# Optimization experiments

Hardware: AMD Instinct MI355X
Metric: run time of the kernel (lower is better)

Reference implementation:

```python
import jax, jax.numpy as jnp
import numpy as np

B, T = 16, 2048
OBS_DIM, ACT_DIM, HIDDEN = 64, 16, 512


def setup_inputs() -> dict:
    key = jax.random.key(0)
    ks = jax.random.split(key, 6)
    n = lambda k, shape, scale: (jax.random.normal(k, shape, dtype=jnp.float32) * scale)
    return {
        "obs": n(ks[0], (B, T, OBS_DIM), 1.0),
        "act": n(ks[1], (B, T, ACT_DIM), 1.0),
        "W_e": n(ks[2], (HIDDEN, OBS_DIM + ACT_DIM), 0.05),   # embed Linear weight
        "b_e": jnp.zeros((HIDDEN,), jnp.float32),             # embed Linear bias
        "a_raw": n(ks[3], (HIDDEN,), 0.5),                    # diagonal decay (pre-tanh)
        "W_B": n(ks[4], (HIDDEN, HIDDEN), 0.02),              # B Linear weight (no bias)
        "W_out": n(ks[5], (OBS_DIM, HIDDEN), 0.04),           # out Linear weight
        "b_out": jnp.zeros((OBS_DIM,), jnp.float32),          # out Linear bias
    }


def reference(obs, act, W_e, b_e, a_raw, W_B, W_out, b_out):
    # x: [B, T, obs+act]
    x = jnp.concatenate([obs, act], axis=-1)
    # embed: Linear + ReLU, batched over all timesteps -> u: [B, T, H]
    u = jax.nn.relu(jnp.einsum('btd,hd->bth', x, W_e) + b_e)
    # B projection batched over all t (the per-step matmul in the torch loop)
    v = jnp.einsum('bth,gh->btg', u, W_B)  # [B, T, H]
    a = jnp.tanh(a_raw)  # [H]
    # Diagonal linear recurrence s_t = a * s_{t-1} + v_t, s_0 starting from zeros,
    # realized as a parallel (log-depth) associative scan over (decay, input) pairs.
    A = jnp.broadcast_to(a, v.shape)
    def combine(c1, c2):
        a1, b1 = c1
        a2, b2 = c2
        return (a1 * a2, a2 * b1 + b2)
    _, s = jax.lax.associative_scan(combine, (A, v), axis=1)  # s: [B, T, H]
    # out projection per step -> preds: [B, T, obs_dim]
    return jnp.einsum('bth,oh->bto', s, W_out) + b_out
```

## Files before the change

kernel.cpp:

```cpp
#include <hip/hip_runtime.h>
#include <hip/hip_bf16.h>

#define B_    16
#define T_    2048
#define H_    512
#define BT_   32768
#define DIN   80
#define DPAD  128
#define L_    64
#define C_    32
#define O_    64
#define NCHUNK (BT_ / L_)

typedef __attribute__((ext_vector_type(8))) short short8;
typedef __attribute__((ext_vector_type(4))) float f32x4;
typedef __attribute__((ext_vector_type(4))) float float4v;

__device__ __forceinline__ float bf2f(unsigned short u) {
  union { unsigned int i; float f; } x; x.i = ((unsigned int)u) << 16; return x.f;
}
__device__ __forceinline__ unsigned short f2bf(float f) {
  union { float f; unsigned int i; } x; x.f = f;
  unsigned int r = x.i + 0x7fffu + ((x.i >> 16) & 1u);
  return (unsigned short)(r >> 16);
}

__global__ __launch_bounds__(512) void gemm_bproj(
    const unsigned short* __restrict__ A, const unsigned short* __restrict__ Bt,
    unsigned short* __restrict__ Cb,
    const float* __restrict__ powa,
    float* __restrict__ e)
{
  constexpr int NT = 8;
  __shared__ __align__(16) unsigned char lds[131072];

  const int tid  = threadIdx.x;
  const int lane = tid & 63;
  const int wid  = tid >> 6;
  const int wr   = wid >> 2;
  const int wc   = wid & 3;
  const int cl   = lane & 15;
  const int kgrp = lane >> 4;
  const int rg   = kgrp * 4;

  const int X  = (int)blockIdx.x & 7;
  const int j  = (int)blockIdx.x >> 3;
  const int mt = X * 16 + (j >> 1);
  const int nt = j & 1;
  const int row0 = mt * 256, col0 = nt * 256;

  auto stageA = [&](int q, int buf) {
    const int k0 = q * 64;
    #pragma unroll
    for (int r = 0; r < 4; ++r) {
      const int o   = r * 8192 + tid * 16;
      const int row = o >> 7;
      const int c16 = (o >> 4) & 7;
      const int kk  = (c16 ^ (row & 7)) << 3;
      __builtin_amdgcn_global_load_lds(
          (const __attribute__((address_space(1))) void*)
              (A + (size_t)(row0 + row) * H_ + k0 + kk),
          (__attribute__((address_space(3))) void*)(lds + buf * 65536 + o),
          16, 0, 0);
    }
  };
  auto stageB_round = [&](int q, int buf, int r) {
    const int k0 = q * 64;
    const int o   = r * 8192 + tid * 16;
    const int col = o >> 7;
    const int c16 = (o >> 4) & 7;
    const int kk  = (c16 ^ (col & 7)) << 3;
    __builtin_amdgcn_global_load_lds(
        (const __attribute__((address_space(1))) void*)
            (Bt + (size_t)(col0 + col) * H_ + k0 + kk),
        (__attribute__((address_space(3))) void*)(lds + buf * 65536 + 32768 + o),
        16, 0, 0);
  };

  f32x4 acc[8][4];
  #pragma unroll
  for (int m = 0; m < 8; ++m)
    #pragma unroll
    for (int n = 0; n < 4; ++n) acc[m][n] = f32x4{0.f, 0.f, 0.f, 0.f};

  stageA(0, 0);
  #pragma unroll
  for (int r = 0; r < 4; ++r) stageB_round(0, 0, r);
  #pragma unroll
  for (int r = 0; r < 4; ++r) stageB_round(1, 1, r);
  asm volatile("s_waitcnt vmcnt(4)" ::: "memory");
  __builtin_amdgcn_sched_barrier(0);
  __builtin_amdgcn_s_barrier();

  for (int q = 0; q < NT; ++q) {
    const int cur = q & 1;
    const unsigned char* bufp = lds + cur * 65536;

    if (q + 1 < NT) stageA(q + 1, cur ^ 1);

    short8 bfr[4][2];
    #pragma unroll
    for (int n = 0; n < 4; ++n) {
      const int col = wc * 64 + n * 16 + cl;
      #pragma unroll
      for (int ks = 0; ks < 2; ++ks)
        bfr[n][ks] = *(const short8*)(bufp + 32768 + col * 128 +
                                      ((((ks << 2) + kgrp) ^ (col & 7)) << 4));
    }
    asm volatile("s_waitcnt lgkmcnt(0)" ::: "memory");
    __builtin_amdgcn_sched_barrier(0);
    __builtin_amdgcn_s_barrier();

    __builtin_amdgcn_s_setprio(1);
    #pragma unroll
    for (int g = 0; g < 4; ++g) {
      if (q + 2 < NT) stageB_round(q + 2, cur, g);
      short8 af[2][2];
      #pragma unroll
      for (int mm = 0; mm < 2; ++mm) {
        const int row = wr * 128 + (g * 2 + mm) * 16 + cl;
        #pragma unroll
        for (int ks = 0; ks < 2; ++ks)
          af[mm][ks] = *(const short8*)(bufp + row * 128 +
                                        ((((ks << 2) + kgrp) ^ (row & 7)) << 4));
      }
      #pragma unroll
      for (int ks = 0; ks < 2; ++ks)
        #pragma unroll
        for (int mm = 0; mm < 2; ++mm)
          #pragma unroll
          for (int n = 0; n < 4; ++n)
            acc[g * 2 + mm][n] = __builtin_amdgcn_mfma_f32_16x16x32_bf16(
                af[mm][ks], bfr[n][ks], acc[g * 2 + mm][n], 0, 0, 0);
    }
    __builtin_amdgcn_s_setprio(0);

    if (q + 2 < NT) {
      asm volatile("s_waitcnt vmcnt(4)" ::: "memory");
    } else if (q + 1 < NT) {
      asm volatile("s_waitcnt vmcnt(0)" ::: "memory");
    }
    __builtin_amdgcn_sched_barrier(0);
    __builtin_amdgcn_s_barrier();
  }

  #pragma unroll
  for (int m = 0; m < 8; ++m) {
    #pragma unroll
    for (int n = 0; n < 4; ++n) {
      const int gc = col0 + wc * 64 + n * 16 + cl;
      #pragma unroll
      for (int e2 = 0; e2 < 4; ++e2) {
        const int gr = row0 + wr * 128 + m * 16 + rg + e2;
        Cb[(size_t)gr * H_ + gc] = f2bf(acc[m][n][e2]);
      }
    }
  }

  #pragma unroll
  for (int c = 0; c < 2; ++c) {
    const int chunk = ((row0 + wr * 128) >> 6) + c;
    #pragma unroll
    for (int n = 0; n < 4; ++n) {
      const int h = col0 + wc * 64 + n * 16 + cl;
      const float a16 = powa[15 * H_ + h];
      float ep = 0.f;
      #pragma unroll
      for (int e2 = 0; e2 < 4; ++e2) {
        const int k = 15 - rg - e2;
        const float wk = (k == 0) ? 1.f : powa[(size_t)(k - 1) * H_ + h];
        float hsum = acc[c * 4 + 0][n][e2];
        hsum = fmaf(hsum, a16, acc[c * 4 + 1][n][e2]);
        hsum = fmaf(hsum, a16, acc[c * 4 + 2][n][e2]);
        hsum = fmaf(hsum, a16, acc[c * 4 + 3][n][e2]);
        ep = fmaf(wk, hsum, ep);
      }
      ep += __shfl_xor(ep, 16);
      ep += __shfl_xor(ep, 32);
      if (kgrp == 0)
        e[(size_t)chunk * H_ + h] = ep;
    }
  }
}

__global__ __launch_bounds__(512) void embed_gemm(
    const float* __restrict__ obs, const float* __restrict__ act,
    const unsigned short* __restrict__ Web,
    const float* __restrict__ b_e,
    unsigned short* __restrict__ u)
{
  __shared__ __align__(16) unsigned char lds[131072];

  const int tid  = threadIdx.x;
  const int lane = tid & 63;
  const int wid  = tid >> 6;
  const int wr   = wid >> 2;
  const int wc   = wid & 3;
  const int cl   = lane & 15;
  const int kgrp = lane >> 4;
  const int rg   = kgrp * 4;

  const int X  = (int)blockIdx.x & 7;
  const int j  = (int)blockIdx.x >> 3;
  const int mt = X * 16 + (j >> 1);
  const int nt = j & 1;
  const int row0 = mt * 256, col0 = nt * 256;

  {
    const int row  = tid >> 1;
    const int half = tid & 1;
    {
      const float4v* src = (const float4v*)(obs + (size_t)(row0 + row) * 64 + half * 32);
      float f[32];
      #pragma unroll
      for (int i = 0; i < 8; ++i) {
        const float4v t4 = src[i];
        f[i*4+0]=t4[0]; f[i*4+1]=t4[1]; f[i*4+2]=t4[2]; f[i*4+3]=t4[3];
      }
      #pragma unroll
      for (int cc = 0; cc < 4; ++cc) {
        short8 o8;
        #pragma unroll
        for (int jj = 0; jj < 8; ++jj) o8[jj] = (short)f2bf(f[cc*8+jj]);
        const int c16 = half * 4 + cc;
        *(short8*)(lds + row * 128 + ((c16 ^ (row & 7)) << 4)) = o8;
      }
    }
    {
      short8 z8;
      #pragma unroll
      for (int jj = 0; jj < 8; ++jj) z8[jj] = 0;
      if (half == 0) {
        const float4v* asrc = (const float4v*)(act + (size_t)(row0 + row) * 16);
        float g[16];
        #pragma unroll
        for (int i = 0; i < 4; ++i) {
          const float4v t4 = asrc[i];
          g[i*4+0]=t4[0]; g[i*4+1]=t4[1]; g[i*4+2]=t4[2]; g[i*4+3]=t4[3];
        }
        #pragma unroll
        for (int cc = 0; cc < 2; ++cc) {
          short8 o8;
          #pragma unroll
          for (int jj = 0; jj < 8; ++jj) o8[jj] = (short)f2bf(g[cc*8+jj]);
          *(short8*)(lds + 65536 + row * 128 + ((cc ^ (row & 7)) << 4)) = o8;
        }
        #pragma unroll
        for (int cc = 2; cc < 4; ++cc)
          *(short8*)(lds + 65536 + row * 128 + ((cc ^ (row & 7)) << 4)) = z8;
      } else {
        #pragma unroll
        for (int cc = 4; cc < 8; ++cc)
          *(short8*)(lds + 65536 + row * 128 + ((cc ^ (row & 7)) << 4)) = z8;
      }
    }
  }
  #pragma unroll
  for (int q = 0; q < 2; ++q) {
    #pragma unroll
    for (int r = 0; r < 4; ++r) {
      const int o   = r * 8192 + tid * 16;
      const int col = o >> 7;
      const int c16 = (o >> 4) & 7;
      const int kk  = (c16 ^ (col & 7)) << 3;
      __builtin_amdgcn_global_load_lds(
          (const __attribute__((address_space(1))) void*)
              (Web + (size_t)(col0 + col) * DPAD + q * 64 + kk),
          (__attribute__((address_space(3))) void*)(lds + q * 65536 + 32768 + o),
          16, 0, 0);
    }
  }
  __syncthreads();

  f32x4 acc[8][4];
  #pragma unroll
  for (int m = 0; m < 8; ++m)
    #pragma unroll
    for (int n = 0; n < 4; ++n) acc[m][n] = f32x4{0.f, 0.f, 0.f, 0.f};

  #pragma unroll
  for (int q = 0; q < 2; ++q) {
    const unsigned char* bufp = lds + q * 65536;
    short8 bfr[4][2];
    #pragma unroll
    for (int n = 0; n < 4; ++n) {
      const int col = wc * 64 + n * 16 + cl;
      #pragma unroll
      for (int ks = 0; ks < 2; ++ks)
        bfr[n][ks] = *(const short8*)(bufp + 32768 + col * 128 +
                                      ((((ks << 2) + kgrp) ^ (col & 7)) << 4));
    }
    #pragma unroll
    for (int g = 0; g < 4; ++g) {
      short8 af[2][2];
      #pragma unroll
      for (int mm = 0; mm < 2; ++mm) {
        const int row = wr * 128 + (g * 2 + mm) * 16 + cl;
        #pragma unroll
        for (int ks = 0; ks < 2; ++ks)
          af[mm][ks] = *(const short8*)(bufp + row * 128 +
                                        ((((ks << 2) + kgrp) ^ (row & 7)) << 4));
      }
      #pragma unroll
      for (int ks = 0; ks < 2; ++ks)
        #pragma unroll
        for (int mm = 0; mm < 2; ++mm)
          #pragma unroll
          for (int n = 0; n < 4; ++n)
            acc[g * 2 + mm][n] = __builtin_amdgcn_mfma_f32_16x16x32_bf16(
                af[mm][ks], bfr[n][ks], acc[g * 2 + mm][n], 0, 0, 0);
    }
  }

  #pragma unroll
  for (int m = 0; m < 8; ++m) {
    #pragma unroll
    for (int n = 0; n < 4; ++n) {
      const int gc = col0 + wc * 64 + n * 16 + cl;
      const float be = b_e[gc];
      #pragma unroll
      for (int e2 = 0; e2 < 4; ++e2) {
        const int gr = row0 + wr * 128 + m * 16 + rg + e2;
        u[(size_t)gr * H_ + gc] = f2bf(fmaxf(acc[m][n][e2] + be, 0.f));
      }
    }
  }
}

#define WE_N  (H_ * DPAD)
#define WB_N  (H_ * H_)
#define WO_N  (O_ * H_)
#define PW_N  (WE_N + WB_N + WO_N + H_)

__global__ __launch_bounds__(256) void prep_w(
    const float* __restrict__ W_e, const float* __restrict__ W_B,
    const float* __restrict__ W_out, const float* __restrict__ a_raw,
    unsigned short* __restrict__ Web, unsigned short* __restrict__ WBb,
    unsigned short* __restrict__ Woutb, float* __restrict__ aarr,
    float* __restrict__ powa)
{
  const int idx = blockIdx.x * 256 + threadIdx.x;
  if (idx < WE_N) {
    const int h = idx >> 7, d = idx & 127;
    Web[idx] = f2bf(d < DIN ? W_e[h * DIN + d] : 0.f);
  } else if (idx < WE_N + WB_N) {
    const int j2 = idx - WE_N;
    WBb[j2] = f2bf(W_B[j2]);
  } else if (idx < WE_N + WB_N + WO_N) {
    const int j2 = idx - (WE_N + WB_N);
    Woutb[j2] = f2bf(W_out[j2]);
  } else if (idx < PW_N) {
    const int h = idx - (WE_N + WB_N + WO_N);
    const float a = tanhf(a_raw[h]);
    aarr[h] = a;
    float p = a;
    #pragma unroll
    for (int i = 0; i < 16; ++i) { powa[i * H_ + h] = p; p *= a; }
  }
}

__global__ __launch_bounds__(256) void carry_scan(
    const float* __restrict__ e, float* __restrict__ P,
    const float* __restrict__ aarr)
{
  const int idx = blockIdx.x * 256 + threadIdx.x;
  const int b = idx >> 9, h = idx & (H_ - 1);
  const float a = aarr[h];
  float aL = a * a; aL *= aL; aL *= aL; aL *= aL; aL *= aL; aL *= aL;
  float ev[C_];
  #pragma unroll
  for (int c = 0; c < C_; ++c)
    ev[c] = e[((size_t)(b * C_ + c)) * H_ + h];
  float S = 0.f;
  #pragma unroll
  for (int c = 0; c < C_; ++c) {
    P[((size_t)(b * C_ + c)) * H_ + h] = S;
    S = fmaf(aL, S, ev[c]);
  }
}

__global__ __launch_bounds__(256) void scan_out(
    const unsigned int* __restrict__ v,
    const float* __restrict__ P,
    const float* __restrict__ aarr,
    const unsigned short* __restrict__ Wo,
    const float* __restrict__ b_out,
    float* __restrict__ y)
{
  __shared__ __align__(16) unsigned char sbytes[64 * 1024];
  const int blk = blockIdx.x;
  const int tid = threadIdx.x;
  const int lane = tid & 63, w = tid >> 6;
  const int row_base = blk * L_;

  {
    const int h0 = tid * 2;
    const float a0 = aarr[h0], a1 = aarr[h0 + 1];
    float s0 = P[(size_t)blk * H_ + h0];
    float s1 = P[(size_t)blk * H_ + h0 + 1];
    const unsigned int* vp = v + (size_t)row_base * (H_ / 2) + tid;
    #pragma unroll 8
    for (int t = 0; t < L_; ++t) {
      const unsigned int pv = vp[(size_t)t * (H_ / 2)];
      s0 = fmaf(a0, s0, bf2f((unsigned short)(pv & 0xffff)));
      s1 = fmaf(a1, s1, bf2f((unsigned short)(pv >> 16)));
      const int byte = t * 1024 + ((tid * 4) ^ ((t & 7) << 4));
      *(unsigned int*)(sbytes + byte) =
          (unsigned int)f2bf(s0) | ((unsigned int)f2bf(s1) << 16);
    }
  }
  __syncthreads();

  f32x4 acc[4];
  #pragma unroll
  for (int n = 0; n < 4; ++n) acc[n] = f32x4{0.f, 0.f, 0.f, 0.f};
  const int r = w * 16 + (lane & 15);
  const int kof = (lane >> 4) * 8;
  #pragma unroll 4
  for (int k0 = 0; k0 < H_; k0 += 32) {
    const int byte = r * 1024 + (((k0 + kof) * 2) ^ ((r & 7) << 4));
    const short8 af = *(const short8*)(sbytes + byte);
    #pragma unroll
    for (int n = 0; n < 4; ++n) {
      const short8 bf = *(const short8*)(Wo + (size_t)(n * 16 + (lane & 15)) * H_ + k0 + kof);
      acc[n] = __builtin_amdgcn_mfma_f32_16x16x32_bf16(af, bf, acc[n], 0, 0, 0);
    }
  }
  const int cl = lane & 15, rg = (lane >> 4) * 4;
  #pragma unroll
  for (int n = 0; n < 4; ++n) {
    #pragma unroll
    for (int e2 = 0; e2 < 4; ++e2) {
      const int gr = row_base + w * 16 + rg + e2;
      const int gc = n * 16 + cl;
      y[(size_t)gr * O_ + gc] = acc[n][e2] + b_out[gc];
    }
  }
}

extern "C" void kernel_launch(void* const* d_in, const int* in_sizes, int n_in,
                              void* d_out, int out_size, void* d_ws, size_t ws_size,
                              hipStream_t stream)
{
  const float* obs   = (const float*)d_in[0];
  const float* act   = (const float*)d_in[1];
  const float* W_e   = (const float*)d_in[2];
  const float* b_e   = (const float*)d_in[3];
  const float* a_raw = (const float*)d_in[4];
  const float* W_B   = (const float*)d_in[5];
  const float* W_out = (const float*)d_in[6];
  const float* b_out = (const float*)d_in[7];
  float* y = (float*)d_out;

  char* w = (char*)d_ws;
  auto carve = [&](size_t bytes) {
    char* p = w; w += (bytes + 255) & ~(size_t)255; return p;
  };
  unsigned short* Web   = (unsigned short*)carve((size_t)H_ * DPAD * 2);
  unsigned short* WBb   = (unsigned short*)carve((size_t)H_ * H_ * 2);
  unsigned short* Woutb = (unsigned short*)carve((size_t)O_ * H_ * 2);
  float*          aarr  = (float*)carve((size_t)H_ * 4);
  float*          powa  = (float*)carve((size_t)16 * H_ * 4);
  unsigned short* u     = (unsigned short*)carve((size_t)BT_ * H_ * 2);
  unsigned short* v     = (unsigned short*)carve((size_t)BT_ * H_ * 2);
  float*          e     = (float*)carve((size_t)NCHUNK * H_ * 4);
  float*          P     = (float*)carve((size_t)NCHUNK * H_ * 4);

  prep_w<<<PW_N / 256, 256, 0, stream>>>(W_e, W_B, W_out, a_raw,
                                         Web, WBb, Woutb, aarr, powa);
  embed_gemm<<<256, 512, 0, stream>>>(obs, act, Web, b_e, u);
  gemm_bproj<<<256, 512, 0, stream>>>(u, WBb, v, powa, e);
  carry_scan<<<(B_ * H_) / 256, 256, 0, stream>>>(e, P, aarr);
  scan_out<<<NCHUNK, 256, 0, stream>>>((const unsigned int*)v, P, aarr,
                                       Woutb, b_out, y);
}
```

Baseline: 70.64 us.

## Fold weight prep into embed GEMM and carry scan into scan_out

Removes the separate prep_w and carry_scan launches. Weight conversion is spread across the embed_gemm blocks, which now load W_e directly from fp32 and convert it into LDS. Each scan_out block recomputes its chunk carry from the per-chunk e values instead of reading a precomputed P. This saves two kernel launches and the P round trip. In exchange, every scan_out block does a redundant serial carry over up to 32 chunks, and embed_gemm does extra conversion work.

```diff
diff --git a/kernel.cpp b/kernel.cpp
--- a/kernel.cpp
+++ b/kernel.cpp
@@ -6,7 +6,6 @@
 #define H_    512
 #define BT_   32768
 #define DIN   80
-#define DPAD  128
 #define L_    64
 #define C_    32
 #define O_    64
@@ -25,11 +24,212 @@
   return (unsigned short)(r >> 16);
 }
 
+#define WB_N  (H_ * H_)
+#define WO_N  (O_ * H_)
+
+__global__ __launch_bounds__(512) void embed_gemm(
+    const float* __restrict__ obs, const float* __restrict__ act,
+    const float* __restrict__ W_e, const float* __restrict__ b_e,
+    const float* __restrict__ a_raw, const float* __restrict__ W_B,
+    const float* __restrict__ W_out,
+    unsigned short* __restrict__ WBb, unsigned short* __restrict__ Woutb,
+    float* __restrict__ aarr, float* __restrict__ powa,
+    unsigned short* __restrict__ u)
+{
+  __shared__ __align__(16) unsigned char lds[131072];
+
+  const int tid  = threadIdx.x;
+  const int lane = tid & 63;
+  const int wid  = tid >> 6;
+  const int wr   = wid >> 2;
+  const int wc   = wid & 3;
+  const int cl   = lane & 15;
+  const int kgrp = lane >> 4;
+  const int rg   = kgrp * 4;
+
+  const int X  = (int)blockIdx.x & 7;
+  const int j  = (int)blockIdx.x >> 3;
+  const int mt = X * 16 + (j >> 1);
+  const int nt = j & 1;
+  const int row0 = mt * 256, col0 = nt * 256;
+
+  {
+    const int g = (int)blockIdx.x * 512 + tid;
+    #pragma unroll
+    for (int r = 0; r < 2; ++r) {
+      const int idx = g * 2 + r;
+      WBb[idx] = f2bf(W_B[idx]);
+    }
+    if (g < WO_N) Woutb[g] = f2bf(W_out[g]);
+    if (g < H_) {
+      const float a = tanhf(a_raw[g]);
+      aarr[g] = a;
+      float p = a;
+      #pragma unroll
+      for (int i = 0; i < 16; ++i) { powa[i * H_ + g] = p; p *= a; }
+    }
+  }
+
+  {
+    const int row  = tid >> 1;
+    const int half = tid & 1;
+    {
+      const float4v* src = (const float4v*)(obs + (size_t)(row0 + row) * 64 + half * 32);
+      float f[32];
+      #pragma unroll
+      for (int i = 0; i < 8; ++i) {
+        const float4v t4 = src[i];
+        f[i*4+0]=t4[0]; f[i*4+1]=t4[1]; f[i*4+2]=t4[2]; f[i*4+3]=t4[3];
+      }
+      #pragma unroll
+      for (int cc = 0; cc < 4; ++cc) {
+        short8 o8;
+        #pragma unroll
+        for (int jj = 0; jj < 8; ++jj) o8[jj] = (short)f2bf(f[cc*8+jj]);
+        const int c16 = half * 4 + cc;
+        *(short8*)(lds + row * 128 + ((c16 ^ (row & 7)) << 4)) = o8;
+      }
+    }
+    {
+      short8 z8;
+      #pragma unroll
+      for (int jj = 0; jj < 8; ++jj) z8[jj] = 0;
+      if (half == 0) {
+        const float4v* asrc = (const float4v*)(act + (size_t)(row0 + row) * 16);
+        float g2[16];
+        #pragma unroll
+        for (int i = 0; i < 4; ++i) {
+          const float4v t4 = asrc[i];
+          g2[i*4+0]=t4[0]; g2[i*4+1]=t4[1]; g2[i*4+2]=t4[2]; g2[i*4+3]=t4[3];
+        }
+        #pragma unroll
+        for (int cc = 0; cc < 2; ++cc) {
+          short8 o8;
+          #pragma unroll
+          for (int jj = 0; jj < 8; ++jj) o8[jj] = (short)f2bf(g2[cc*8+jj]);
+          *(short8*)(lds + 65536 + row * 128 + ((cc ^ (row & 7)) << 4)) = o8;
+        }
+        #pragma unroll
+        for (int cc = 2; cc < 4; ++cc)
+          *(short8*)(lds + 65536 + row * 128 + ((cc ^ (row & 7)) << 4)) = z8;
+      } else {
+        #pragma unroll
+        for (int cc = 4; cc < 8; ++cc)
+          *(short8*)(lds + 65536 + row * 128 + ((cc ^ (row & 7)) << 4)) = z8;
+      }
+    }
+  }
+  {
+    const int colL = tid >> 1;
+    const int col  = col0 + colL;
+    const int half = tid & 1;
+    {
+      const float4v* src = (const float4v*)(W_e + (size_t)col * DIN + half * 32);
+      float f[32];
+      #pragma unroll
+      for (int i = 0; i < 8; ++i) {
+        const float4v t4 = src[i];
+        f[i*4+0]=t4[0]; f[i*4+1]=t4[1]; f[i*4+2]=t4[2]; f[i*4+3]=t4[3];
+      }
+      #pragma unroll
+      for (int cc = 0; cc < 4; ++cc) {
+        short8 o8;
+        #pragma unroll
+        for (int jj = 0; jj < 8; ++jj) o8[jj] = (short)f2bf(f[cc*8+jj]);
+        const int c16 = half * 4 + cc;
+        *(short8*)(lds + 32768 + colL * 128 + ((c16 ^ (colL & 7)) << 4)) = o8;
+      }
+    }
+    {
+      short8 z8;
+      #pragma unroll
+      for (int jj = 0; jj < 8; ++jj) z8[jj] = 0;
+      if (half == 0) {
+        const float4v* src = (const float4v*)(W_e + (size_t)col * DIN + 64);
+        float g2[16];
+        #pragma unroll
+        for (int i = 0; i < 4; ++i) {
+          const float4v t4 = src[i];
+          g2[i*4+0]=t4[0]; g2[i*4+1]=t4[1]; g2[i*4+2]=t4[2]; g2[i*4+3]=t4[3];
+        }
+        #pragma unroll
+        for (int cc = 0; cc < 2; ++cc) {
+          short8 o8;
+          #pragma unroll
+          for (int jj = 0; jj < 8; ++jj) o8[jj] = (short)f2bf(g2[cc*8+jj]);
+          *(short8*)(lds + 98304 + colL * 128 + ((cc ^ (colL & 7)) << 4)) = o8;
+        }
+        #pragma unroll
+        for (int cc = 2; cc < 4; ++cc)
+          *(short8*)(lds + 98304 + colL * 128 + ((cc ^ (colL & 7)) << 4)) = z8;
+      } else {
+        #pragma unroll
+        for (int cc = 4; cc < 8; ++cc)
+          *(short8*)(lds + 98304 + colL * 128 + ((cc ^ (colL & 7)) << 4)) = z8;
+      }
+    }
+  }
+  __syncthreads();
+
+  f32x4 acc[8][4];
+  #pragma unroll
+  for (int m = 0; m < 8; ++m)
+    #pragma unroll
+    for (int n = 0; n < 4; ++n) acc[m][n] = f32x4{0.f, 0.f, 0.f, 0.f};
+
+  #pragma unroll
+  for (int q = 0; q < 2; ++q) {
+    const unsigned char* bufp = lds + q * 65536;
+    short8 bfr[4][2];
+    #pragma unroll
+    for (int n = 0; n < 4; ++n) {
+      const int col = wc * 64 + n * 16 + cl;
+      #pragma unroll
+      for (int ks = 0; ks < 2; ++ks)
+        bfr[n][ks] = *(const short8*)(bufp + 32768 + col * 128 +
+                                      ((((ks << 2) + kgrp) ^ (col & 7)) << 4));
+    }
+    #pragma unroll
+    for (int g = 0; g < 4; ++g) {
+      short8 af[2][2];
+      #pragma unroll
+      for (int mm = 0; mm < 2; ++mm) {
+        const int row = wr * 128 + (g * 2 + mm) * 16 + cl;
+        #pragma unroll
+        for (int ks = 0; ks < 2; ++ks)
+          af[mm][ks] = *(const short8*)(bufp + row * 128 +
+                                        ((((ks << 2) + kgrp) ^ (row & 7)) << 4));
+      }
+      #pragma unroll
+      for (int ks = 0; ks < 2; ++ks)
+        #pragma unroll
+        for (int mm = 0; mm < 2; ++mm)
+          #pragma unroll
+          for (int n = 0; n < 4; ++n)
+            acc[g * 2 + mm][n] = __builtin_amdgcn_mfma_f32_16x16x32_bf16(
+                af[mm][ks], bfr[n][ks], acc[g * 2 + mm][n], 0, 0, 0);
+    }
+  }
+
+  #pragma unroll
+  for (int m = 0; m < 8; ++m) {
+    #pragma unroll
+    for (int n = 0; n < 4; ++n) {
+      const int gc = col0 + wc * 64 + n * 16 + cl;
+      const float be = b_e[gc];
+      #pragma unroll
+      for (int e2 = 0; e2 < 4; ++e2) {
+        const int gr = row0 + wr * 128 + m * 16 + rg + e2;
+        u[(size_t)gr * H_ + gc] = f2bf(fmaxf(acc[m][n][e2] + be, 0.f));
+      }
+    }
+  }
+}
+
 __global__ __launch_bounds__(512) void gemm_bproj(
     const unsigned short* __restrict__ A, const unsigned short* __restrict__ Bt,
     unsigned short* __restrict__ Cb,
-    const float* __restrict__ powa,
-    float* __restrict__ e)
+    const float* __restrict__ powa, float* __restrict__ e)
 {
   constexpr int NT = 8;
   __shared__ __align__(16) unsigned char lds[131072];
@@ -183,212 +383,14 @@
   }
 }
 
-__global__ __launch_bounds__(512) void embed_gemm(
-    const float* __restrict__ obs, const float* __restrict__ act,
-    const unsigned short* __restrict__ Web,
-    const float* __restrict__ b_e,
-    unsigned short* __restrict__ u)
-{
-  __shared__ __align__(16) unsigned char lds[131072];
-
-  const int tid  = threadIdx.x;
-  const int lane = tid & 63;
-  const int wid  = tid >> 6;
-  const int wr   = wid >> 2;
-  const int wc   = wid & 3;
-  const int cl   = lane & 15;
-  const int kgrp = lane >> 4;
-  const int rg   = kgrp * 4;
-
-  const int X  = (int)blockIdx.x & 7;
-  const int j  = (int)blockIdx.x >> 3;
-  const int mt = X * 16 + (j >> 1);
-  const int nt = j & 1;
-  const int row0 = mt * 256, col0 = nt * 256;
-
-  {
-    const int row  = tid >> 1;
-    const int half = tid & 1;
-    {
-      const float4v* src = (const float4v*)(obs + (size_t)(row0 + row) * 64 + half * 32);
-      float f[32];
-      #pragma unroll
-      for (int i = 0; i < 8; ++i) {
-        const float4v t4 = src[i];
-        f[i*4+0]=t4[0]; f[i*4+1]=t4[1]; f[i*4+2]=t4[2]; f[i*4+3]=t4[3];
-      }
-      #pragma unroll
-      for (int cc = 0; cc < 4; ++cc) {
-        short8 o8;
-        #pragma unroll
-        for (int jj = 0; jj < 8; ++jj) o8[jj] = (short)f2bf(f[cc*8+jj]);
-        const int c16 = half * 4 + cc;
-        *(short8*)(lds + row * 128 + ((c16 ^ (row & 7)) << 4)) = o8;
-      }
-    }
-    {
-      short8 z8;
-      #pragma unroll
-      for (int jj = 0; jj < 8; ++jj) z8[jj] = 0;
-      if (half == 0) {
-        const float4v* asrc = (const float4v*)(act + (size_t)(row0 + row) * 16);
-        float g[16];
-        #pragma unroll
-        for (int i = 0; i < 4; ++i) {
-          const float4v t4 = asrc[i];
-          g[i*4+0]=t4[0]; g[i*4+1]=t4[1]; g[i*4+2]=t4[2]; g[i*4+3]=t4[3];
-        }
-        #pragma unroll
-        for (int cc = 0; cc < 2; ++cc) {
-          short8 o8;
-          #pragma unroll
-          for (int jj = 0; jj < 8; ++jj) o8[jj] = (short)f2bf(g[cc*8+jj]);
-          *(short8*)(lds + 65536 + row * 128 + ((cc ^ (row & 7)) << 4)) = o8;
-        }
-        #pragma unroll
-        for (int cc = 2; cc < 4; ++cc)
-          *(short8*)(lds + 65536 + row * 128 + ((cc ^ (row & 7)) << 4)) = z8;
-      } else {
-        #pragma unroll
-        for (int cc = 4; cc < 8; ++cc)
-          *(short8*)(lds + 65536 + row * 128 + ((cc ^ (row & 7)) << 4)) = z8;
-      }
-    }
-  }
-  #pragma unroll
-  for (int q = 0; q < 2; ++q) {
-    #pragma unroll
-    for (int r = 0; r < 4; ++r) {
-      const int o   = r * 8192 + tid * 16;
-      const int col = o >> 7;
-      const int c16 = (o >> 4) & 7;
-      const int kk  = (c16 ^ (col & 7)) << 3;
-      __builtin_amdgcn_global_load_lds(
-          (const __attribute__((address_space(1))) void*)
-              (Web + (size_t)(col0 + col) * DPAD + q * 64 + kk),
-          (__attribute__((address_space(3))) void*)(lds + q * 65536 + 32768 + o),
-          16, 0, 0);
-    }
-  }
-  __syncthreads();
-
-  f32x4 acc[8][4];
-  #pragma unroll
-  for (int m = 0; m < 8; ++m)
-    #pragma unroll
-    for (int n = 0; n < 4; ++n) acc[m][n] = f32x4{0.f, 0.f, 0.f, 0.f};
-
-  #pragma unroll
-  for (int q = 0; q < 2; ++q) {
-    const unsigned char* bufp = lds + q * 65536;
-    short8 bfr[4][2];
-    #pragma unroll
-    for (int n = 0; n < 4; ++n) {
-      const int col = wc * 64 + n * 16 + cl;
-      #pragma unroll
-      for (int ks = 0; ks < 2; ++ks)
-        bfr[n][ks] = *(const short8*)(bufp + 32768 + col * 128 +
-                                      ((((ks << 2) + kgrp) ^ (col & 7)) << 4));
-    }
-    #pragma unroll
-    for (int g = 0; g < 4; ++g) {
-      short8 af[2][2];
-      #pragma unroll
-      for (int mm = 0; mm < 2; ++mm) {
-        const int row = wr * 128 + (g * 2 + mm) * 16 + cl;
-        #pragma unroll
-        for (int ks = 0; ks < 2; ++ks)
-          af[mm][ks] = *(const short8*)(bufp + row * 128 +
-                                        ((((ks << 2) + kgrp) ^ (row & 7)) << 4));
-      }
-      #pragma unroll
-      for (int ks = 0; ks < 2; ++ks)
-        #pragma unroll
-        for (int mm = 0; mm < 2; ++mm)
-          #pragma unroll
-          for (int n = 0; n < 4; ++n)
-            acc[g * 2 + mm][n] = __builtin_amdgcn_mfma_f32_16x16x32_bf16(
-                af[mm][ks], bfr[n][ks], acc[g * 2 + mm][n], 0, 0, 0);
-    }
-  }
-
-  #pragma unroll
-  for (int m = 0; m < 8; ++m) {
-    #pragma unroll
-    for (int n = 0; n < 4; ++n) {
-      const int gc = col0 + wc * 64 + n * 16 + cl;
-      const float be = b_e[gc];
-      #pragma unroll
-      for (int e2 = 0; e2 < 4; ++e2) {
-        const int gr = row0 + wr * 128 + m * 16 + rg + e2;
-        u[(size_t)gr * H_ + gc] = f2bf(fmaxf(acc[m][n][e2] + be, 0.f));
-      }
-    }
-  }
-}
-
-#define WE_N  (H_ * DPAD)
-#define WB_N  (H_ * H_)
-#define WO_N  (O_ * H_)
-#define PW_N  (WE_N + WB_N + WO_N + H_)
-
-__global__ __launch_bounds__(256) void prep_w(
-    const float* __restrict__ W_e, const float* __restrict__ W_B,
-    const float* __restrict__ W_out, const float* __restrict__ a_raw,
-    unsigned short* __restrict__ Web, unsigned short* __restrict__ WBb,
-    unsigned short* __restrict__ Woutb, float* __restrict__ aarr,
-    float* __restrict__ powa)
-{
-  const int idx = blockIdx.x * 256 + threadIdx.x;
-  if (idx < WE_N) {
-    const int h = idx >> 7, d = idx & 127;
-    Web[idx] = f2bf(d < DIN ? W_e[h * DIN + d] : 0.f);
-  } else if (idx < WE_N + WB_N) {
-    const int j2 = idx - WE_N;
-    WBb[j2] = f2bf(W_B[j2]);
-  } else if (idx < WE_N + WB_N + WO_N) {
-    const int j2 = idx - (WE_N + WB_N);
-    Woutb[j2] = f2bf(W_out[j2]);
-  } else if (idx < PW_N) {
-    const int h = idx - (WE_N + WB_N + WO_N);
-    const float a = tanhf(a_raw[h]);
-    aarr[h] = a;
-    float p = a;
-    #pragma unroll
-    for (int i = 0; i < 16; ++i) { powa[i * H_ + h] = p; p *= a; }
-  }
-}
-
-__global__ __launch_bounds__(256) void carry_scan(
-    const float* __restrict__ e, float* __restrict__ P,
-    const float* __restrict__ aarr)
-{
-  const int idx = blockIdx.x * 256 + threadIdx.x;
-  const int b = idx >> 9, h = idx & (H_ - 1);
-  const float a = aarr[h];
-  float aL = a * a; aL *= aL; aL *= aL; aL *= aL; aL *= aL; aL *= aL;
-  float ev[C_];
-  #pragma unroll
-  for (int c = 0; c < C_; ++c)
-    ev[c] = e[((size_t)(b * C_ + c)) * H_ + h];
-  float S = 0.f;
-  #pragma unroll
-  for (int c = 0; c < C_; ++c) {
-    P[((size_t)(b * C_ + c)) * H_ + h] = S;
-    S = fmaf(aL, S, ev[c]);
-  }
-}
-
 __global__ __launch_bounds__(256) void scan_out(
-    const unsigned int* __restrict__ v,
-    const float* __restrict__ P,
-    const float* __restrict__ aarr,
-    const unsigned short* __restrict__ Wo,
-    const float* __restrict__ b_out,
-    float* __restrict__ y)
+    const unsigned int* __restrict__ v, const float* __restrict__ e,
+    const float* __restrict__ aarr, const unsigned short* __restrict__ Wo,
+    const float* __restrict__ b_out, float* __restrict__ y)
 {
   __shared__ __align__(16) unsigned char sbytes[64 * 1024];
   const int blk = blockIdx.x;
+  const int b = blk >> 5, c = blk & 31;
   const int tid = threadIdx.x;
   const int lane = tid & 63, w = tid >> 6;
   const int row_base = blk * L_;
@@ -396,8 +398,28 @@
   {
     const int h0 = tid * 2;
     const float a0 = aarr[h0], a1 = aarr[h0 + 1];
-    float s0 = P[(size_t)blk * H_ + h0];
-    float s1 = P[(size_t)blk * H_ + h0 + 1];
+    float aL0 = a0 * a0, aL1 = a1 * a1;
+    aL0 *= aL0; aL1 *= aL1;
+    aL0 *= aL0; aL1 *= aL1;
+    aL0 *= aL0; aL1 *= aL1;
+    aL0 *= aL0; aL1 *= aL1;
+    aL0 *= aL0; aL1 *= aL1;
+    float s0 = 0.f, s1 = 0.f;
+    #pragma unroll
+    for (int g = 0; g < 4; ++g) {
+      float ev0[8], ev1[8];
+      #pragma unroll
+      for (int k = 0; k < 8; ++k) {
+        const size_t o = ((size_t)(b * C_ + g * 8 + k)) * H_ + h0;
+        ev0[k] = e[o]; ev1[k] = e[o + 1];
+      }
+      #pragma unroll
+      for (int k = 0; k < 8; ++k) {
+        const bool pred = (g * 8 + k) < c;
+        s0 = pred ? fmaf(aL0, s0, ev0[k]) : s0;
+        s1 = pred ? fmaf(aL1, s1, ev1[k]) : s1;
+      }
+    }
     const unsigned int* vp = v + (size_t)row_base * (H_ / 2) + tid;
     #pragma unroll 8
     for (int t = 0; t < L_; ++t) {
@@ -456,7 +478,6 @@
   auto carve = [&](size_t bytes) {
     char* p = w; w += (bytes + 255) & ~(size_t)255; return p;
   };
-  unsigned short* Web   = (unsigned short*)carve((size_t)H_ * DPAD * 2);
   unsigned short* WBb   = (unsigned short*)carve((size_t)H_ * H_ * 2);
   unsigned short* Woutb = (unsigned short*)carve((size_t)O_ * H_ * 2);
   float*          aarr  = (float*)carve((size_t)H_ * 4);
@@ -464,13 +485,10 @@
   unsigned short* u     = (unsigned short*)carve((size_t)BT_ * H_ * 2);
   unsigned short* v     = (unsigned short*)carve((size_t)BT_ * H_ * 2);
   float*          e     = (float*)carve((size_t)NCHUNK * H_ * 4);
-  float*          P     = (float*)carve((size_t)NCHUNK * H_ * 4);
-
-  prep_w<<<PW_N / 256, 256, 0, stream>>>(W_e, W_B, W_out, a_raw,
-                                         Web, WBb, Woutb, aarr, powa);
-  embed_gemm<<<256, 512, 0, stream>>>(obs, act, Web, b_e, u);
+
+  embed_gemm<<<256, 512, 0, stream>>>(obs, act, W_e, b_e, a_raw, W_B, W_out,
+                                      WBb, Woutb, aarr, powa, u);
   gemm_bproj<<<256, 512, 0, stream>>>(u, WBb, v, powa, e);
-  carry_scan<<<(B_ * H_) / 256, 256, 0, stream>>>(e, P, aarr);
-  scan_out<<<NCHUNK, 256, 0, stream>>>((const unsigned int*)v, P, aarr,
+  scan_out<<<NCHUNK, 256, 0, stream>>>((const unsigned int*)v, e, aarr,
                                        Woutb, b_out, y);
 }
```

Result: faster. 68.21 us (-3.4%).

## Fuse embed and B-projection GEMMs, fold carry scan into scan_out

Applied to the files above, without the earlier changes.

Merges the embed GEMM and the B projection into one kernel. Each K-slice of the ReLU embedding is computed into LDS and consumed directly by the B-projection MFMAs, so the u intermediate never goes to global memory. The carry_scan kernel is removed: each scan_out block recomputes its chunk carry from the per-chunk e sums with a predicated serial loop. The block index is also remapped for locality. In exchange, the embed work is recomputed by both column-tile blocks, W_B is now read straight from global memory instead of through async LDS staging, and the carry recompute adds redundant work in scan_out.

```diff
diff --git a/kernel.cpp b/kernel.cpp
--- a/kernel.cpp
+++ b/kernel.cpp
@@ -6,7 +6,6 @@
 #define H_    512
 #define BT_   32768
 #define DIN   80
-#define DPAD  128
 #define L_    64
 #define C_    32
 #define O_    64
@@ -25,309 +24,8 @@
   return (unsigned short)(r >> 16);
 }
 
-__global__ __launch_bounds__(512) void gemm_bproj(
-    const unsigned short* __restrict__ A, const unsigned short* __restrict__ Bt,
-    unsigned short* __restrict__ Cb,
-    const float* __restrict__ powa,
-    float* __restrict__ e)
-{
-  constexpr int NT = 8;
-  __shared__ __align__(16) unsigned char lds[131072];
-
-  const int tid  = threadIdx.x;
-  const int lane = tid & 63;
-  const int wid  = tid >> 6;
-  const int wr   = wid >> 2;
-  const int wc   = wid & 3;
-  const int cl   = lane & 15;
-  const int kgrp = lane >> 4;
-  const int rg   = kgrp * 4;
-
-  const int X  = (int)blockIdx.x & 7;
-  const int j  = (int)blockIdx.x >> 3;
-  const int mt = X * 16 + (j >> 1);
-  const int nt = j & 1;
-  const int row0 = mt * 256, col0 = nt * 256;
-
-  auto stageA = [&](int q, int buf) {
-    const int k0 = q * 64;
-    #pragma unroll
-    for (int r = 0; r < 4; ++r) {
-      const int o   = r * 8192 + tid * 16;
-      const int row = o >> 7;
-      const int c16 = (o >> 4) & 7;
-      const int kk  = (c16 ^ (row & 7)) << 3;
-      __builtin_amdgcn_global_load_lds(
-          (const __attribute__((address_space(1))) void*)
-              (A + (size_t)(row0 + row) * H_ + k0 + kk),
-          (__attribute__((address_space(3))) void*)(lds + buf * 65536 + o),
-          16, 0, 0);
-    }
-  };
-  auto stageB_round = [&](int q, int buf, int r) {
-    const int k0 = q * 64;
-    const int o   = r * 8192 + tid * 16;
-    const int col = o >> 7;
-    const int c16 = (o >> 4) & 7;
-    const int kk  = (c16 ^ (col & 7)) << 3;
-    __builtin_amdgcn_global_load_lds(
-        (const __attribute__((address_space(1))) void*)
-            (Bt + (size_t)(col0 + col) * H_ + k0 + kk),
-        (__attribute__((address_space(3))) void*)(lds + buf * 65536 + 32768 + o),
-        16, 0, 0);
-  };
-
-  f32x4 acc[8][4];
-  #pragma unroll
-  for (int m = 0; m < 8; ++m)
-    #pragma unroll
-    for (int n = 0; n < 4; ++n) acc[m][n] = f32x4{0.f, 0.f, 0.f, 0.f};
-
-  stageA(0, 0);
-  #pragma unroll
-  for (int r = 0; r < 4; ++r) stageB_round(0, 0, r);
-  #pragma unroll
-  for (int r = 0; r < 4; ++r) stageB_round(1, 1, r);
-  asm volatile("s_waitcnt vmcnt(4)" ::: "memory");
-  __builtin_amdgcn_sched_barrier(0);
-  __builtin_amdgcn_s_barrier();
-
-  for (int q = 0; q < NT; ++q) {
-    const int cur = q & 1;
-    const unsigned char* bufp = lds + cur * 65536;
-
-    if (q + 1 < NT) stageA(q + 1, cur ^ 1);
-
-    short8 bfr[4][2];
-    #pragma unroll
-    for (int n = 0; n < 4; ++n) {
-      const int col = wc * 64 + n * 16 + cl;
-      #pragma unroll
-      for (int ks = 0; ks < 2; ++ks)
-        bfr[n][ks] = *(const short8*)(bufp + 32768 + col * 128 +
-                                      ((((ks << 2) + kgrp) ^ (col & 7)) << 4));
-    }
-    asm volatile("s_waitcnt lgkmcnt(0)" ::: "memory");
-    __builtin_amdgcn_sched_barrier(0);
-    __builtin_amdgcn_s_barrier();
-
-    __builtin_amdgcn_s_setprio(1);
-    #pragma unroll
-    for (int g = 0; g < 4; ++g) {
-      if (q + 2 < NT) stageB_round(q + 2, cur, g);
-      short8 af[2][2];
-      #pragma unroll
-      for (int mm = 0; mm < 2; ++mm) {
-        const int row = wr * 128 + (g * 2 + mm) * 16 + cl;
-        #pragma unroll
-        for (int ks = 0; ks < 2; ++ks)
-          af[mm][ks] = *(const short8*)(bufp + row * 128 +
-                                        ((((ks << 2) + kgrp) ^ (row & 7)) << 4));
-      }
-      #pragma unroll
-      for (int ks = 0; ks < 2; ++ks)
-        #pragma unroll
-        for (int mm = 0; mm < 2; ++mm)
-          #pragma unroll
-          for (int n = 0; n < 4; ++n)
-            acc[g * 2 + mm][n] = __builtin_amdgcn_mfma_f32_16x16x32_bf16(
-                af[mm][ks], bfr[n][ks], acc[g * 2 + mm][n], 0, 0, 0);
-    }
-    __builtin_amdgcn_s_setprio(0);
-
-    if (q + 2 < NT) {
-      asm volatile("s_waitcnt vmcnt(4)" ::: "memory");
-    } else if (q + 1 < NT) {
-      asm volatile("s_waitcnt vmcnt(0)" ::: "memory");
-    }
-    __builtin_amdgcn_sched_barrier(0);
-    __builtin_amdgcn_s_barrier();
-  }
-
-  #pragma unroll
-  for (int m = 0; m < 8; ++m) {
-    #pragma unroll
-    for (int n = 0; n < 4; ++n) {
-      const int gc = col0 + wc * 64 + n * 16 + cl;
-      #pragma unroll
-      for (int e2 = 0; e2 < 4; ++e2) {
-        const int gr = row0 + wr * 128 + m * 16 + rg + e2;
-        Cb[(size_t)gr * H_ + gc] = f2bf(acc[m][n][e2]);
-      }
-    }
-  }
-
-  #pragma unroll
-  for (int c = 0; c < 2; ++c) {
-    const int chunk = ((row0 + wr * 128) >> 6) + c;
-    #pragma unroll
-    for (int n = 0; n < 4; ++n) {
-      const int h = col0 + wc * 64 + n * 16 + cl;
-      const float a16 = powa[15 * H_ + h];
-      float ep = 0.f;
-      #pragma unroll
-      for (int e2 = 0; e2 < 4; ++e2) {
-        const int k = 15 - rg - e2;
-        const float wk = (k == 0) ? 1.f : powa[(size_t)(k - 1) * H_ + h];
-        float hsum = acc[c * 4 + 0][n][e2];
-        hsum = fmaf(hsum, a16, acc[c * 4 + 1][n][e2]);
-        hsum = fmaf(hsum, a16, acc[c * 4 + 2][n][e2]);
-        hsum = fmaf(hsum, a16, acc[c * 4 + 3][n][e2]);
-        ep = fmaf(wk, hsum, ep);
-      }
-      ep += __shfl_xor(ep, 16);
-      ep += __shfl_xor(ep, 32);
-      if (kgrp == 0)
-        e[(size_t)chunk * H_ + h] = ep;
-    }
-  }
-}
-
-__global__ __launch_bounds__(512) void embed_gemm(
-    const float* __restrict__ obs, const float* __restrict__ act,
-    const unsigned short* __restrict__ Web,
-    const float* __restrict__ b_e,
-    unsigned short* __restrict__ u)
-{
-  __shared__ __align__(16) unsigned char lds[131072];
-
-  const int tid  = threadIdx.x;
-  const int lane = tid & 63;
-  const int wid  = tid >> 6;
-  const int wr   = wid >> 2;
-  const int wc   = wid & 3;
-  const int cl   = lane & 15;
-  const int kgrp = lane >> 4;
-  const int rg   = kgrp * 4;
-
-  const int X  = (int)blockIdx.x & 7;
-  const int j  = (int)blockIdx.x >> 3;
-  const int mt = X * 16 + (j >> 1);
-  const int nt = j & 1;
-  const int row0 = mt * 256, col0 = nt * 256;
-
-  {
-    const int row  = tid >> 1;
-    const int half = tid & 1;
-    {
-      const float4v* src = (const float4v*)(obs + (size_t)(row0 + row) * 64 + half * 32);
-      float f[32];
-      #pragma unroll
-      for (int i = 0; i < 8; ++i) {
-        const float4v t4 = src[i];
-        f[i*4+0]=t4[0]; f[i*4+1]=t4[1]; f[i*4+2]=t4[2]; f[i*4+3]=t4[3];
-      }
-      #pragma unroll
-      for (int cc = 0; cc < 4; ++cc) {
-        short8 o8;
-        #pragma unroll
-        for (int jj = 0; jj < 8; ++jj) o8[jj] = (short)f2bf(f[cc*8+jj]);
-        const int c16 = half * 4 + cc;
-        *(short8*)(lds + row * 128 + ((c16 ^ (row & 7)) << 4)) = o8;
-      }
-    }
-    {
-      short8 z8;
-      #pragma unroll
-      for (int jj = 0; jj < 8; ++jj) z8[jj] = 0;
-      if (half == 0) {
-        const float4v* asrc = (const float4v*)(act + (size_t)(row0 + row) * 16);
-        float g[16];
-        #pragma unroll
-        for (int i = 0; i < 4; ++i) {
-          const float4v t4 = asrc[i];
-          g[i*4+0]=t4[0]; g[i*4+1]=t4[1]; g[i*4+2]=t4[2]; g[i*4+3]=t4[3];
-        }
-        #pragma unroll
-        for (int cc = 0; cc < 2; ++cc) {
-          short8 o8;
-          #pragma unroll
-          for (int jj = 0; jj < 8; ++jj) o8[jj] = (short)f2bf(g[cc*8+jj]);
-          *(short8*)(lds + 65536 + row * 128 + ((cc ^ (row & 7)) << 4)) = o8;
-        }
-        #pragma unroll
-        for (int cc = 2; cc < 4; ++cc)
-          *(short8*)(lds + 65536 + row * 128 + ((cc ^ (row & 7)) << 4)) = z8;
-      } else {
-        #pragma unroll
-        for (int cc = 4; cc < 8; ++cc)
-          *(short8*)(lds + 65536 + row * 128 + ((cc ^ (row & 7)) << 4)) = z8;
-      }
-    }
-  }
-  #pragma unroll
-  for (int q = 0; q < 2; ++q) {
-    #pragma unroll
-    for (int r = 0; r < 4; ++r) {
-      const int o   = r * 8192 + tid * 16;
-      const int col = o >> 7;
-      const int c16 = (o >> 4) & 7;
-      const int kk  = (c16 ^ (col & 7)) << 3;
-      __builtin_amdgcn_global_load_lds(
-          (const __attribute__((address_space(1))) void*)
-              (Web + (size_t)(col0 + col) * DPAD + q * 64 + kk),
-          (__attribute__((address_space(3))) void*)(lds + q * 65536 + 32768 + o),
-          16, 0, 0);
-    }
-  }
-  __syncthreads();
-
-  f32x4 acc[8][4];
-  #pragma unroll
-  for (int m = 0; m < 8; ++m)
-    #pragma unroll
-    for (int n = 0; n < 4; ++n) acc[m][n] = f32x4{0.f, 0.f, 0.f, 0.f};
-
-  #pragma unroll
-  for (int q = 0; q < 2; ++q) {
-    const unsigned char* bufp = lds + q * 65536;
-    short8 bfr[4][2];
-    #pragma unroll
-    for (int n = 0; n < 4; ++n) {
-      const int col = wc * 64 + n * 16 + cl;
-      #pragma unroll
-      for (int ks = 0; ks < 2; ++ks)
-        bfr[n][ks] = *(const short8*)(bufp + 32768 + col * 128 +
-                                      ((((ks << 2) + kgrp) ^ (col & 7)) << 4));
-    }
-    #pragma unroll
-    for (int g = 0; g < 4; ++g) {
-      short8 af[2][2];
-      #pragma unroll
-      for (int mm = 0; mm < 2; ++mm) {
-        const int row = wr * 128 + (g * 2 + mm) * 16 + cl;
-        #pragma unroll
-        for (int ks = 0; ks < 2; ++ks)
-          af[mm][ks] = *(const short8*)(bufp + row * 128 +
-                                        ((((ks << 2) + kgrp) ^ (row & 7)) << 4));
-      }
-      #pragma unroll
-      for (int ks = 0; ks < 2; ++ks)
-        #pragma unroll
-        for (int mm = 0; mm < 2; ++mm)
-          #pragma unroll
-          for (int n = 0; n < 4; ++n)
-            acc[g * 2 + mm][n] = __builtin_amdgcn_mfma_f32_16x16x32_bf16(
-                af[mm][ks], bfr[n][ks], acc[g * 2 + mm][n], 0, 0, 0);
-    }
-  }
-
-  #pragma unroll
-  for (int m = 0; m < 8; ++m) {
-    #pragma unroll
-    for (int n = 0; n < 4; ++n) {
-      const int gc = col0 + wc * 64 + n * 16 + cl;
-      const float be = b_e[gc];
-      #pragma unroll
-      for (int e2 = 0; e2 < 4; ++e2) {
-        const int gr = row0 + wr * 128 + m * 16 + rg + e2;
-        u[(size_t)gr * H_ + gc] = f2bf(fmaxf(acc[m][n][e2] + be, 0.f));
-      }
-    }
-  }
-}
-
-#define WE_N  (H_ * DPAD)
+#define WEP   96
+#define WE_N  (H_ * WEP)
 #define WB_N  (H_ * H_)
 #define WO_N  (O_ * H_)
 #define PW_N  (WE_N + WB_N + WO_N + H_)
@@ -341,8 +39,8 @@
 {
   const int idx = blockIdx.x * 256 + threadIdx.x;
   if (idx < WE_N) {
-    const int h = idx >> 7, d = idx & 127;
-    Web[idx] = f2bf(d < DIN ? W_e[h * DIN + d] : 0.f);
+    const int h = idx / WEP, d = idx % WEP;
+    Web[idx] = (d < DIN) ? f2bf(W_e[h * DIN + d]) : (unsigned short)0;
   } else if (idx < WE_N + WB_N) {
     const int j2 = idx - WE_N;
     WBb[j2] = f2bf(W_B[j2]);
@@ -359,36 +57,221 @@
   }
 }
 
-__global__ __launch_bounds__(256) void carry_scan(
-    const float* __restrict__ e, float* __restrict__ P,
-    const float* __restrict__ aarr)
+__global__ __launch_bounds__(512) void fused_eb(
+    const float* __restrict__ obs, const float* __restrict__ act,
+    const unsigned short* __restrict__ Web,
+    const float* __restrict__ b_e,
+    const unsigned short* __restrict__ WBb,
+    const float* __restrict__ powa,
+    unsigned short* __restrict__ v, float* __restrict__ e)
 {
-  const int idx = blockIdx.x * 256 + threadIdx.x;
-  const int b = idx >> 9, h = idx & (H_ - 1);
-  const float a = aarr[h];
-  float aL = a * a; aL *= aL; aL *= aL; aL *= aL; aL *= aL; aL *= aL;
-  float ev[C_];
-  #pragma unroll
-  for (int c = 0; c < C_; ++c)
-    ev[c] = e[((size_t)(b * C_ + c)) * H_ + h];
-  float S = 0.f;
-  #pragma unroll
-  for (int c = 0; c < C_; ++c) {
-    P[((size_t)(b * C_ + c)) * H_ + h] = S;
-    S = fmaf(aL, S, ev[c]);
+  __shared__ __align__(16) unsigned char lds[131072];
+
+  const int tid  = threadIdx.x;
+  const int lane = tid & 63;
+  const int wid  = tid >> 6;
+  const int wr   = wid >> 2;
+  const int wc   = wid & 3;
+  const int cl   = lane & 15;
+  const int kgrp = lane >> 4;
+  const int rg   = kgrp * 4;
+
+  const int X  = (int)blockIdx.x & 7;
+  const int j  = (int)blockIdx.x >> 3;
+  const int mt = X * 16 + (j >> 1);
+  const int nt = j & 1;
+  const int row0 = mt * 256, col0 = nt * 256;
+
+  {
+    const int row  = tid >> 1;
+    const int half = tid & 1;
+    {
+      const float4v* src = (const float4v*)(obs + (size_t)(row0 + row) * 64 + half * 32);
+      float f[32];
+      #pragma unroll
+      for (int i = 0; i < 8; ++i) {
+        const float4v t4 = src[i];
+        f[i*4+0]=t4[0]; f[i*4+1]=t4[1]; f[i*4+2]=t4[2]; f[i*4+3]=t4[3];
+      }
+      #pragma unroll
+      for (int cc = 0; cc < 4; ++cc) {
+        short8 o8;
+        #pragma unroll
+        for (int jj = 0; jj < 8; ++jj) o8[jj] = (short)f2bf(f[cc*8+jj]);
+        const int c16 = half * 4 + cc;
+        *(short8*)(lds + row * 256 + ((c16 ^ (row & 15)) << 4)) = o8;
+      }
+    }
+    if (half == 0) {
+      const float4v* asrc = (const float4v*)(act + (size_t)(row0 + row) * 16);
+      float g2[16];
+      #pragma unroll
+      for (int i = 0; i < 4; ++i) {
+        const float4v t4 = asrc[i];
+        g2[i*4+0]=t4[0]; g2[i*4+1]=t4[1]; g2[i*4+2]=t4[2]; g2[i*4+3]=t4[3];
+      }
+      #pragma unroll
+      for (int cc = 0; cc < 2; ++cc) {
+        short8 o8;
+        #pragma unroll
+        for (int jj = 0; jj < 8; ++jj) o8[jj] = (short)f2bf(g2[cc*8+jj]);
+        *(short8*)(lds + row * 256 + (((8 + cc) ^ (row & 15)) << 4)) = o8;
+      }
+      short8 z8;
+      #pragma unroll
+      for (int jj = 0; jj < 8; ++jj) z8[jj] = 0;
+      #pragma unroll
+      for (int cc = 2; cc < 4; ++cc)
+        *(short8*)(lds + row * 256 + (((8 + cc) ^ (row & 15)) << 4)) = z8;
+    }
+  }
+  __syncthreads();
+
+  auto embed_phase = [&](int q, int buf) {
+    const int k0 = q * 64;
+    short8 wb[4][3];
+    #pragma unroll
+    for (int nF = 0; nF < 4; ++nF) {
+      const int h = k0 + nF * 16 + cl;
+      #pragma unroll
+      for (int kxs = 0; kxs < 3; ++kxs)
+        wb[nF][kxs] = *(const short8*)(Web + (size_t)h * WEP + kxs * 32 + kgrp * 8);
+    }
+    short8 xa[2][3];
+    #pragma unroll
+    for (int mF = 0; mF < 2; ++mF) {
+      const int row = (wid << 5) + mF * 16 + cl;
+      #pragma unroll
+      for (int kxs = 0; kxs < 3; ++kxs) {
+        const int c16 = kxs * 4 + kgrp;
+        xa[mF][kxs] = *(const short8*)(lds + row * 256 + ((c16 ^ (row & 15)) << 4));
+      }
+    }
+    f32x4 ea[2][4];
+    #pragma unroll
+    for (int mF = 0; mF < 2; ++mF)
+      #pragma unroll
+      for (int nF = 0; nF < 4; ++nF) ea[mF][nF] = f32x4{0.f, 0.f, 0.f, 0.f};
+    #pragma unroll
+    for (int kxs = 0; kxs < 3; ++kxs)
+      #pragma unroll
+      for (int mF = 0; mF < 2; ++mF)
+        #pragma unroll
+        for (int nF = 0; nF < 4; ++nF)
+          ea[mF][nF] = __builtin_amdgcn_mfma_f32_16x16x32_bf16(
+              xa[mF][kxs], wb[nF][kxs], ea[mF][nF], 0, 0, 0);
+    unsigned char* abuf = lds + 65536 + buf * 32768;
+    #pragma unroll
+    for (int nF = 0; nF < 4; ++nF) {
+      const int colL = nF * 16 + cl;
+      const float be = b_e[k0 + colL];
+      const int c16 = colL >> 3;
+      const int cb  = (colL & 7) * 2;
+      #pragma unroll
+      for (int mF = 0; mF < 2; ++mF) {
+        #pragma unroll
+        for (int e2 = 0; e2 < 4; ++e2) {
+          const int row = (wid << 5) + mF * 16 + rg + e2;
+          const float uu = fmaxf(ea[mF][nF][e2] + be, 0.f);
+          *(unsigned short*)(abuf + row * 128 + ((c16 ^ (row & 7)) << 4) + cb) = f2bf(uu);
+        }
+      }
+    }
+  };
+
+  f32x4 acc[8][4];
+  #pragma unroll
+  for (int m = 0; m < 8; ++m)
+    #pragma unroll
+    for (int n = 0; n < 4; ++n) acc[m][n] = f32x4{0.f, 0.f, 0.f, 0.f};
+
+  embed_phase(0, 0);
+  __syncthreads();
+
+  for (int q = 0; q < 8; ++q) {
+    if (q + 1 < 8) embed_phase(q + 1, (q + 1) & 1);
+
+    const unsigned char* bufp = lds + 65536 + (q & 1) * 32768;
+    short8 bfr[4][2];
+    #pragma unroll
+    for (int nF = 0; nF < 4; ++nF) {
+      const int col = col0 + wc * 64 + nF * 16 + cl;
+      #pragma unroll
+      for (int ks = 0; ks < 2; ++ks)
+        bfr[nF][ks] = *(const short8*)(WBb + (size_t)col * H_ + q * 64 + ks * 32 + kgrp * 8);
+    }
+    __builtin_amdgcn_s_setprio(1);
+    #pragma unroll
+    for (int g = 0; g < 4; ++g) {
+      short8 af[2][2];
+      #pragma unroll
+      for (int mm = 0; mm < 2; ++mm) {
+        const int row = wr * 128 + (g * 2 + mm) * 16 + cl;
+        #pragma unroll
+        for (int ks = 0; ks < 2; ++ks)
+          af[mm][ks] = *(const short8*)(bufp + row * 128 +
+                                        ((((ks << 2) + kgrp) ^ (row & 7)) << 4));
+      }
+      #pragma unroll
+      for (int ks = 0; ks < 2; ++ks)
+        #pragma unroll
+        for (int mm = 0; mm < 2; ++mm)
+          #pragma unroll
+          for (int n = 0; n < 4; ++n)
+            acc[g * 2 + mm][n] = __builtin_amdgcn_mfma_f32_16x16x32_bf16(
+                af[mm][ks], bfr[n][ks], acc[g * 2 + mm][n], 0, 0, 0);
+    }
+    __builtin_amdgcn_s_setprio(0);
+    __syncthreads();
+  }
+
+  #pragma unroll
+  for (int m = 0; m < 8; ++m) {
+    #pragma unroll
+    for (int n = 0; n < 4; ++n) {
+      const int gc = col0 + wc * 64 + n * 16 + cl;
+      #pragma unroll
+      for (int e2 = 0; e2 < 4; ++e2) {
+        const int gr = row0 + wr * 128 + m * 16 + rg + e2;
+        v[(size_t)gr * H_ + gc] = f2bf(acc[m][n][e2]);
+      }
+    }
+  }
+
+  #pragma unroll
+  for (int c = 0; c < 2; ++c) {
+    const int chunk = ((row0 + wr * 128) >> 6) + c;
+    #pragma unroll
+    for (int n = 0; n < 4; ++n) {
+      const int h = col0 + wc * 64 + n * 16 + cl;
+      const float a16 = powa[15 * H_ + h];
+      float ep = 0.f;
+      #pragma unroll
+      for (int e2 = 0; e2 < 4; ++e2) {
+        const int k = 15 - rg - e2;
+        const float wk = (k == 0) ? 1.f : powa[(size_t)(k - 1) * H_ + h];
+        float hsum = acc[c * 4 + 0][n][e2];
+        hsum = fmaf(hsum, a16, acc[c * 4 + 1][n][e2]);
+        hsum = fmaf(hsum, a16, acc[c * 4 + 2][n][e2]);
+        hsum = fmaf(hsum, a16, acc[c * 4 + 3][n][e2]);
+        ep = fmaf(wk, hsum, ep);
+      }
+      ep += __shfl_xor(ep, 16);
+      ep += __shfl_xor(ep, 32);
+      if (kgrp == 0)
+        e[(size_t)chunk * H_ + h] = ep;
+    }
   }
 }
 
 __global__ __launch_bounds__(256) void scan_out(
-    const unsigned int* __restrict__ v,
-    const float* __restrict__ P,
-    const float* __restrict__ aarr,
-    const unsigned short* __restrict__ Wo,
-    const float* __restrict__ b_out,
-    float* __restrict__ y)
+    const unsigned int* __restrict__ v, const float* __restrict__ e,
+    const float* __restrict__ aarr, const unsigned short* __restrict__ Wo,
+    const float* __restrict__ b_out, float* __restrict__ y)
 {
   __shared__ __align__(16) unsigned char sbytes[64 * 1024];
-  const int blk = blockIdx.x;
+  const int blk = ((int)blockIdx.x & 7) * 64 + ((int)blockIdx.x >> 3);
+  const int b = blk >> 5, c = blk & 31;
   const int tid = threadIdx.x;
   const int lane = tid & 63, w = tid >> 6;
   const int row_base = blk * L_;
@@ -396,8 +279,28 @@
   {
     const int h0 = tid * 2;
     const float a0 = aarr[h0], a1 = aarr[h0 + 1];
-    float s0 = P[(size_t)blk * H_ + h0];
-    float s1 = P[(size_t)blk * H_ + h0 + 1];
+    float aL0 = a0 * a0, aL1 = a1 * a1;
+    aL0 *= aL0; aL1 *= aL1;
+    aL0 *= aL0; aL1 *= aL1;
+    aL0 *= aL0; aL1 *= aL1;
+    aL0 *= aL0; aL1 *= aL1;
+    aL0 *= aL0; aL1 *= aL1;
+    float s0 = 0.f, s1 = 0.f;
+    #pragma unroll
+    for (int g = 0; g < 4; ++g) {
+      float ev0[8], ev1[8];
+      #pragma unroll
+      for (int k = 0; k < 8; ++k) {
+        const size_t o = ((size_t)(b * C_ + g * 8 + k)) * H_ + h0;
+        ev0[k] = e[o]; ev1[k] = e[o + 1];
+      }
+      #pragma unroll
+      for (int k = 0; k < 8; ++k) {
+        const bool pred = (g * 8 + k) < c;
+        s0 = pred ? fmaf(aL0, s0, ev0[k]) : s0;
+        s1 = pred ? fmaf(aL1, s1, ev1[k]) : s1;
+      }
+    }
     const unsigned int* vp = v + (size_t)row_base * (H_ / 2) + tid;
     #pragma unroll 8
     for (int t = 0; t < L_; ++t) {
@@ -456,21 +359,17 @@
   auto carve = [&](size_t bytes) {
     char* p = w; w += (bytes + 255) & ~(size_t)255; return p;
   };
-  unsigned short* Web   = (unsigned short*)carve((size_t)H_ * DPAD * 2);
+  unsigned short* Web   = (unsigned short*)carve((size_t)H_ * WEP * 2);
   unsigned short* WBb   = (unsigned short*)carve((size_t)H_ * H_ * 2);
   unsigned short* Woutb = (unsigned short*)carve((size_t)O_ * H_ * 2);
   float*          aarr  = (float*)carve((size_t)H_ * 4);
   float*          powa  = (float*)carve((size_t)16 * H_ * 4);
-  unsigned short* u     = (unsigned short*)carve((size_t)BT_ * H_ * 2);
   unsigned short* v     = (unsigned short*)carve((size_t)BT_ * H_ * 2);
   float*          e     = (float*)carve((size_t)NCHUNK * H_ * 4);
-  float*          P     = (float*)carve((size_t)NCHUNK * H_ * 4);
 
   prep_w<<<PW_N / 256, 256, 0, stream>>>(W_e, W_B, W_out, a_raw,
                                          Web, WBb, Woutb, aarr, powa);
-  embed_gemm<<<256, 512, 0, stream>>>(obs, act, Web, b_e, u);
-  gemm_bproj<<<256, 512, 0, stream>>>(u, WBb, v, powa, e);
-  carry_scan<<<(B_ * H_) / 256, 256, 0, stream>>>(e, P, aarr);
-  scan_out<<<NCHUNK, 256, 0, stream>>>((const unsigned int*)v, P, aarr,
+  fused_eb<<<256, 512, 0, stream>>>(obs, act, Web, b_e, WBb, powa, v, e);
+  scan_out<<<NCHUNK, 256, 0, stream>>>((const unsigned int*)v, e, aarr,
                                        Woutb, b_out, y);
 }
```

Result: slower. 82.63 us (+17.0%).
